# Performance work log

Measured on AMD Instinct MI355X. Metric: run time of the kernel, lower is better.

Reference implementation:

```python
import jax, jax.numpy as jnp
import numpy as np

B = 64          # batch
NV = 6890       # SMPL vertices
NF = 13776      # SMPL faces
NHD = 20000     # HD (uniformly resampled) vertices
NP = 24         # SMPL parts
COP_W = 10.0
COP_K = 100.0
EPS = 1e-6


def setup_inputs() -> dict:
    key = jax.random.key(0)
    k1, k2, k3, k4, k5 = jax.random.split(key, 5)
    vertices = jax.random.normal(k1, (B, NV, 3), jnp.float32)
    hd_operator = jax.random.uniform(k2, (NHD, NV), jnp.float32) / NV
    faces = jax.random.randint(k3, (NF, 3), 0, NV)          # triangle vertex ids
    vert_fid = jax.random.randint(k4, (NHD,), 0, NF)        # HD vert -> source face
    face_part = jax.random.randint(k5, (NF,), 0, NP)        # face -> body part
    return {"vertices": vertices, "hd_operator": hd_operator,
            "faces": faces, "vert_fid": vert_fid, "face_part": face_part}


def reference(vertices, hd_operator, faces, vert_fid, face_part):
    # --- per-part volume: signed tetrahedron volume per face, summed per part ---
    tri = vertices[:, faces]                      # [B, NF, 3, 3]
    v0, v1, v2 = tri[:, :, 0], tri[:, :, 1], tri[:, :, 2]
    vol_f = jnp.abs(jnp.einsum('bfi,bfi->bf', v0, jnp.cross(v1, v2))) / 6.0  # [B, NF]
    part_onehot = jax.nn.one_hot(face_part, NP, dtype=vol_f.dtype)           # [NF, NP]
    per_part_volume = jnp.einsum('bf,fp->bp', vol_f, part_onehot)            # [B, NP]

    vertices_hd = jnp.einsum('nm,bmd->bnd', hd_operator, vertices)           # [B, NHD, 3]

    # --- map each HD vertex to the volume of its part ---
    part_of_vert = face_part[vert_fid]                                       # [NHD]
    vol_vert = per_part_volume[:, part_of_vert][..., None]                   # [B, NHD, 1]

    # --- volume-weighted COM ---
    com = jnp.sum(vertices_hd * vol_vert, axis=1) / jnp.sum(vol_vert, axis=1)  # [B, 3]

    # --- pressure-weighted COP ---
    h = vertices_hd[:, :, 1]  # vertex height above ground plane (y)
    pw = jnp.where(h < 0.0, 1.0 - COP_K * h, jnp.exp(-COP_W * h))            # [B, NHD]
    cop = jnp.sum(vertices_hd * pw[..., None], axis=1) / (
        jnp.sum(pw, axis=1, keepdims=True) + EPS)                            # [B, 3]

    # --- stability loss: xz distance between COM and COP ---
    d = com - cop
    return jnp.sqrt(d[:, 0] ** 2 + d[:, 2] ** 2)                             # [B]
```

## Files before the change

kernel.cpp:

```cpp
#include <hip/hip_runtime.h>
#include <cstdint>

#define B_    64
#define NV_   6890
#define NF_   13776
#define NHD_  20000
#define NP_   24
#define NCH   216
#define BUF_HW 6144

#define OFF_PPV   0u
#define OFF_RED   6144u
#define OFF_VC    7680u

typedef __attribute__((ext_vector_type(8))) __bf16 bf16x8;
typedef __attribute__((ext_vector_type(4))) float f32x4;

__device__ __forceinline__ unsigned short f2bf(float f) {
    unsigned u = __float_as_uint(f);
    u = (u + 0x7fffu + ((u >> 16) & 1u)) >> 16;
    return (unsigned short)u;
}

__global__ __launch_bounds__(256) void k_init(float* __restrict__ z) {
    for (int i = threadIdx.x; i < 1920; i += 256) z[i] = 0.f;
}

__global__ __launch_bounds__(256) void k0v_pack(const float* __restrict__ verts,
                                                unsigned short* __restrict__ Vc) {
    int idx = blockIdx.x * 256 + threadIdx.x;
    int j    = idx & 7;
    int lane = (idx >> 3) & 63;
    int ct   = idx >> 9;
    int t    = ct % 12;
    int c    = ct / 12;
    int lm   = lane & 15;
    int kk   = (lane >> 4) * 8 + j;
    int bd   = t * 16 + lm;
    int d    = bd >> 6, b = bd & 63;
    int k    = c * 32 + kk;
    float v  = (k < NV_) ? verts[((size_t)b * NV_ + k) * 3 + d] : 0.f;
    Vc[idx] = f2bf(v);
}

__global__ __launch_bounds__(256) void k1_vol(const float* __restrict__ verts,
                                              const int* __restrict__ faces,
                                              const int* __restrict__ face_part,
                                              float* __restrict__ ppv) {
    __shared__ float bins[NP_];
    int b = blockIdx.y;
    int f = blockIdx.x * 256 + threadIdx.x;
    if (threadIdx.x < NP_) bins[threadIdx.x] = 0.f;
    __syncthreads();
    if (f < NF_) {
        int i0 = faces[3 * f], i1 = faces[3 * f + 1], i2 = faces[3 * f + 2];
        const float* vb = verts + (size_t)b * NV_ * 3;
        float ax = vb[3 * i0], ay = vb[3 * i0 + 1], az = vb[3 * i0 + 2];
        float bx = vb[3 * i1], by = vb[3 * i1 + 1], bz = vb[3 * i1 + 2];
        float cx = vb[3 * i2], cy = vb[3 * i2 + 1], cz = vb[3 * i2 + 2];
        float crx = by * cz - bz * cy;
        float cry = bz * cx - bx * cz;
        float crz = bx * cy - by * cx;
        float vol = fabsf(ax * crx + ay * cry + az * crz) * (1.0f / 6.0f);
        atomicAdd(&bins[face_part[f]], vol);
    }
    __syncthreads();
    if (threadIdx.x < NP_) atomicAdd(&ppv[b * NP_ + threadIdx.x], bins[threadIdx.x]);
}

__global__ __launch_bounds__(64) void kf_fused(const float* __restrict__ Hm,
                                               const unsigned short* __restrict__ Vc,
                                               const int* __restrict__ vert_fid,
                                               const int* __restrict__ face_part,
                                               const float* __restrict__ ppv,
                                               float* __restrict__ red) {
    __shared__ unsigned short Vl[2 * BUF_HW];
    const int lane = threadIdx.x;
    const int lm   = lane & 15;
    const int kg   = lane >> 4;
    const int n0   = blockIdx.x * 32;
    const float* Arow0 = Hm + (size_t)(n0 + lm) * NV_;
    const float* Arow1 = Hm + (size_t)(n0 + 16 + lm) * NV_;

    f32x4 acc0[12], acc1[12];
#pragma unroll
    for (int t = 0; t < 12; ++t) {
        acc0[t] = (f32x4){0.f, 0.f, 0.f, 0.f};
        acc1[t] = (f32x4){0.f, 0.f, 0.f, 0.f};
    }

    auto stage = [&](int cc, unsigned short* dst) {
        const unsigned short* src = Vc + (size_t)cc * BUF_HW + lane * 8;
#pragma unroll
        for (int i = 0; i < 12; ++i)
            __builtin_amdgcn_global_load_lds(
                (const __attribute__((address_space(1))) void*)(src + i * 512),
                (__attribute__((address_space(3))) void*)(dst + i * 512), 16, 0, 0);
    };
    auto loadA = [&](int cc, float2* ra, float2* rb) {
        int k0 = cc * 32 + kg * 8;
#pragma unroll
        for (int j = 0; j < 4; ++j) {
            ra[j] = *reinterpret_cast<const float2*>(Arow0 + k0 + 2 * j);
            rb[j] = *reinterpret_cast<const float2*>(Arow1 + k0 + 2 * j);
        }
    };

    stage(0, &Vl[0]);
    float2 a[4], b[4];
    loadA(0, a, b);

    int p = 0;
#pragma unroll 1
    for (int c = 0; c < NCH - 1; ++c) {
        asm volatile("s_waitcnt vmcnt(0)" ::: "memory");
        __builtin_amdgcn_sched_barrier(0);
        bf16x8 Af0, Af1;
#pragma unroll
        for (int j = 0; j < 4; ++j) {
            Af0[2 * j]     = (__bf16)a[j].x;
            Af0[2 * j + 1] = (__bf16)a[j].y;
            Af1[2 * j]     = (__bf16)b[j].x;
            Af1[2 * j + 1] = (__bf16)b[j].y;
        }
        __builtin_amdgcn_sched_barrier(0);
        stage(c + 1, &Vl[(p ^ 1) * BUF_HW]);
        int cpf = (c + 1 < NCH - 1) ? (c + 1) : (NCH - 2);
        loadA(cpf, a, b);
        __builtin_amdgcn_sched_barrier(0);
        bf16x8 Bu[12];
        const unsigned short* bp = &Vl[p * BUF_HW] + lane * 8;
#pragma unroll
        for (int t = 0; t < 12; ++t)
            Bu[t] = *reinterpret_cast<const bf16x8*>(bp + t * 512);
#pragma unroll
        for (int t = 0; t < 12; ++t)
            acc0[t] = __builtin_amdgcn_mfma_f32_16x16x32_bf16(Af0, Bu[t], acc0[t], 0, 0, 0);
#pragma unroll
        for (int t = 0; t < 12; ++t)
            acc1[t] = __builtin_amdgcn_mfma_f32_16x16x32_bf16(Af1, Bu[t], acc1[t], 0, 0, 0);
        p ^= 1;
    }

    {
        asm volatile("s_waitcnt vmcnt(0)" ::: "memory");
        __builtin_amdgcn_sched_barrier(0);
        bf16x8 Bu[12];
        const unsigned short* bp = &Vl[p * BUF_HW] + lane * 8;
#pragma unroll
        for (int t = 0; t < 12; ++t)
            Bu[t] = *reinterpret_cast<const bf16x8*>(bp + t * 512);
        int k0 = (NCH - 1) * 32 + kg * 8;
        bf16x8 Af0, Af1;
#pragma unroll
        for (int j = 0; j < 8; ++j) {
            int k = k0 + j;
            float fa = (k < NV_) ? Arow0[k] : 0.f;
            float fb = (k < NV_) ? Arow1[k] : 0.f;
            Af0[j] = (__bf16)fa;
            Af1[j] = (__bf16)fb;
        }
#pragma unroll
        for (int t = 0; t < 12; ++t)
            acc0[t] = __builtin_amdgcn_mfma_f32_16x16x32_bf16(Af0, Bu[t], acc0[t], 0, 0, 0);
#pragma unroll
        for (int t = 0; t < 12; ++t)
            acc1[t] = __builtin_amdgcn_mfma_f32_16x16x32_bf16(Af1, Bu[t], acc1[t], 0, 0, 0);
    }

    int part0[4], part1[4];
#pragma unroll
    for (int r = 0; r < 4; ++r) {
        part0[r] = face_part[vert_fid[n0 + kg * 4 + r]];
        part1[r] = face_part[vert_fid[n0 + 16 + kg * 4 + r]];
    }
    float sums[4][6];
#pragma unroll
    for (int t = 0; t < 4; ++t)
#pragma unroll
        for (int q = 0; q < 6; ++q) sums[t][q] = 0.f;

#pragma unroll
    for (int t = 0; t < 4; ++t) {
        int bcol = t * 16 + lm;
#pragma unroll
        for (int r = 0; r < 4; ++r) {
            {
                float x = acc0[t][r], h = acc0[4 + t][r], z = acc0[8 + t][r];
                float pwv = (h < 0.f) ? (1.f - 100.f * h) : expf(-10.f * h);
                float w = ppv[bcol * NP_ + part0[r]];
                sums[t][0] += pwv * x; sums[t][1] += pwv * z;
                sums[t][2] += w * x;   sums[t][3] += w * z;
                sums[t][4] += pwv;     sums[t][5] += w;
            }
            {
                float x = acc1[t][r], h = acc1[4 + t][r], z = acc1[8 + t][r];
                float pwv = (h < 0.f) ? (1.f - 100.f * h) : expf(-10.f * h);
                float w = ppv[bcol * NP_ + part1[r]];
                sums[t][0] += pwv * x; sums[t][1] += pwv * z;
                sums[t][2] += w * x;   sums[t][3] += w * z;
                sums[t][4] += pwv;     sums[t][5] += w;
            }
        }
    }
#pragma unroll
    for (int t = 0; t < 4; ++t)
#pragma unroll
        for (int q = 0; q < 6; ++q) {
            float v = sums[t][q];
            v += __shfl_xor(v, 16);
            v += __shfl_xor(v, 32);
            sums[t][q] = v;
        }
    if (kg == 0) {
#pragma unroll
        for (int t = 0; t < 4; ++t) {
            int bcol = t * 16 + lm;
#pragma unroll
            for (int q = 0; q < 6; ++q)
                atomicAdd(&red[bcol * 6 + q], sums[t][q]);
        }
    }
}

__global__ __launch_bounds__(64) void k5_final(const float* __restrict__ red,
                                               float* __restrict__ out) {
    int b = threadIdx.x;
    if (b < B_) {
        float sp   = red[b * 6 + 4] + 1e-6f;
        float sw   = red[b * 6 + 5];
        float copx = red[b * 6 + 0] / sp;
        float copz = red[b * 6 + 1] / sp;
        float comx = red[b * 6 + 2] / sw;
        float comz = red[b * 6 + 3] / sw;
        float dx = comx - copx, dz = comz - copz;
        out[b] = sqrtf(dx * dx + dz * dz);
    }
}

extern "C" void kernel_launch(void* const* d_in, const int* in_sizes, int n_in,
                              void* d_out, int out_size, void* d_ws, size_t ws_size,
                              hipStream_t stream) {
    const float* verts     = (const float*)d_in[0];
    const float* Hm        = (const float*)d_in[1];
    const int*   faces     = (const int*)d_in[2];
    const int*   vert_fid  = (const int*)d_in[3];
    const int*   face_part = (const int*)d_in[4];
    char* ws = (char*)d_ws;
    float*          ppv = (float*)(ws + OFF_PPV);
    float*          red = (float*)(ws + OFF_RED);
    unsigned short* Vc  = (unsigned short*)(ws + OFF_VC);
    float* out = (float*)d_out;

    hipLaunchKernelGGL(k_init, dim3(1), dim3(256), 0, stream, (float*)ws);
    hipLaunchKernelGGL(k0v_pack, dim3((NCH * 12 * 512) / 256), dim3(256), 0, stream, verts, Vc);
    hipLaunchKernelGGL(k1_vol, dim3(54, 64), dim3(256), 0, stream, verts, faces, face_part, ppv);
    hipLaunchKernelGGL(kf_fused, dim3(NHD_ / 32), dim3(64), 0, stream,
                       Hm, Vc, vert_fid, face_part, ppv, red);
    hipLaunchKernelGGL(k5_final, dim3(1), dim3(64), 0, stream, red, out);
}
```

Baseline: 361.1 us.

## Use 4-wave blocks with split-K and shared B tiles in fused regressor GEMM

The fused HD-regressor kernel now launches 256-thread blocks of four waves. Two waves cover 64 output rows and share the staged vertex tiles in LDS, each loading half of them. The other pair splits the K dimension in half, and the two halves' accumulators are reduced through LDS before the epilogue. This is meant to shorten each wave's serial K loop, raise the number of memory requests in flight per CU, and cut redundant B staging. In exchange it adds block-wide barriers every iteration, an LDS reduction step, and bounds masking for the partial last block.

```diff
diff --git a/kernel.cpp b/kernel.cpp
--- a/kernel.cpp
+++ b/kernel.cpp
@@ -7,6 +7,7 @@
 #define NHD_  20000
 #define NP_   24
 #define NCH   216
+#define ITERS 108
 #define BUF_HW 6144
 
 #define OFF_PPV   0u
@@ -68,19 +69,27 @@
     if (threadIdx.x < NP_) atomicAdd(&ppv[b * NP_ + threadIdx.x], bins[threadIdx.x]);
 }
 
-__global__ __launch_bounds__(64) void kf_fused(const float* __restrict__ Hm,
-                                               const unsigned short* __restrict__ Vc,
-                                               const int* __restrict__ vert_fid,
-                                               const int* __restrict__ face_part,
-                                               const float* __restrict__ ppv,
-                                               float* __restrict__ red) {
-    __shared__ unsigned short Vl[2 * BUF_HW];
-    const int lane = threadIdx.x;
+__global__ __launch_bounds__(256) void kf_fused(const float* __restrict__ Hm,
+                                                const unsigned short* __restrict__ Vc,
+                                                const int* __restrict__ vert_fid,
+                                                const int* __restrict__ face_part,
+                                                const float* __restrict__ ppv,
+                                                float* __restrict__ red) {
+    __shared__ unsigned short Vb[2][2][BUF_HW];
+    const int tid  = threadIdx.x;
+    const int lane = tid & 63;
+    const int w    = tid >> 6;
+    const int wr   = w & 1;
+    const int ws   = w >> 1;
     const int lm   = lane & 15;
     const int kg   = lane >> 4;
-    const int n0   = blockIdx.x * 32;
-    const float* Arow0 = Hm + (size_t)(n0 + lm) * NV_;
-    const float* Arow1 = Hm + (size_t)(n0 + 16 + lm) * NV_;
+    const int n0   = blockIdx.x * 64;
+    const int rowbase = n0 + 32 * wr;
+    const int r0c = min(rowbase + lm,      NHD_ - 1);
+    const int r1c = min(rowbase + 16 + lm, NHD_ - 1);
+    const float* Arow0 = Hm + (size_t)r0c * NV_;
+    const float* Arow1 = Hm + (size_t)r1c * NV_;
+    const int cbase = ws * ITERS;
 
     f32x4 acc0[12], acc1[12];
 #pragma unroll
@@ -89,31 +98,55 @@
         acc1[t] = (f32x4){0.f, 0.f, 0.f, 0.f};
     }
 
-    auto stage = [&](int cc, unsigned short* dst) {
-        const unsigned short* src = Vc + (size_t)cc * BUF_HW + lane * 8;
-#pragma unroll
-        for (int i = 0; i < 12; ++i)
+    auto stageTiles = [&](int cc, int pp) {
+        const unsigned short* src = Vc + (size_t)cc * BUF_HW;
+        unsigned short* dst = &Vb[ws][pp][0];
+#pragma unroll
+        for (int i = 0; i < 6; ++i) {
+            int t = wr * 6 + i;
             __builtin_amdgcn_global_load_lds(
-                (const __attribute__((address_space(1))) void*)(src + i * 512),
-                (__attribute__((address_space(3))) void*)(dst + i * 512), 16, 0, 0);
+                (const __attribute__((address_space(1))) void*)(src + t * 512 + lane * 8),
+                (__attribute__((address_space(3))) void*)(dst + t * 512 + lane * 8), 16, 0, 0);
+        }
     };
     auto loadA = [&](int cc, float2* ra, float2* rb) {
         int k0 = cc * 32 + kg * 8;
-#pragma unroll
-        for (int j = 0; j < 4; ++j) {
-            ra[j] = *reinterpret_cast<const float2*>(Arow0 + k0 + 2 * j);
-            rb[j] = *reinterpret_cast<const float2*>(Arow1 + k0 + 2 * j);
+        if (cc == NCH - 1) {
+            float ta[8], tb[8];
+#pragma unroll
+            for (int j = 0; j < 8; ++j) {
+                int k = k0 + j;
+                ta[j] = (k < NV_) ? Arow0[k] : 0.f;
+                tb[j] = (k < NV_) ? Arow1[k] : 0.f;
+            }
+#pragma unroll
+            for (int j = 0; j < 4; ++j) {
+                ra[j] = make_float2(ta[2 * j], ta[2 * j + 1]);
+                rb[j] = make_float2(tb[2 * j], tb[2 * j + 1]);
+            }
+        } else {
+#pragma unroll
+            for (int j = 0; j < 4; ++j) {
+                ra[j] = *reinterpret_cast<const float2*>(Arow0 + k0 + 2 * j);
+                rb[j] = *reinterpret_cast<const float2*>(Arow1 + k0 + 2 * j);
+            }
         }
     };
 
-    stage(0, &Vl[0]);
+    stageTiles(cbase, 0);
     float2 a[4], b[4];
-    loadA(0, a, b);
+    loadA(cbase, a, b);
+    __syncthreads();
 
     int p = 0;
 #pragma unroll 1
-    for (int c = 0; c < NCH - 1; ++c) {
-        asm volatile("s_waitcnt vmcnt(0)" ::: "memory");
+    for (int i = 0; i < ITERS; ++i) {
+        const int c = cbase + i;
+        bf16x8 Bu[12];
+        const unsigned short* bp = &Vb[ws][p][0] + lane * 8;
+#pragma unroll
+        for (int t = 0; t < 12; ++t)
+            Bu[t] = *reinterpret_cast<const bf16x8*>(bp + t * 512);
         __builtin_amdgcn_sched_barrier(0);
         bf16x8 Af0, Af1;
 #pragma unroll
@@ -124,101 +157,90 @@
             Af1[2 * j + 1] = (__bf16)b[j].y;
         }
         __builtin_amdgcn_sched_barrier(0);
-        stage(c + 1, &Vl[(p ^ 1) * BUF_HW]);
-        int cpf = (c + 1 < NCH - 1) ? (c + 1) : (NCH - 2);
-        loadA(cpf, a, b);
+        if (i + 1 < ITERS) stageTiles(c + 1, p ^ 1);
+        loadA((i + 1 < ITERS) ? c + 1 : c, a, b);
         __builtin_amdgcn_sched_barrier(0);
-        bf16x8 Bu[12];
-        const unsigned short* bp = &Vl[p * BUF_HW] + lane * 8;
-#pragma unroll
-        for (int t = 0; t < 12; ++t)
-            Bu[t] = *reinterpret_cast<const bf16x8*>(bp + t * 512);
 #pragma unroll
         for (int t = 0; t < 12; ++t)
             acc0[t] = __builtin_amdgcn_mfma_f32_16x16x32_bf16(Af0, Bu[t], acc0[t], 0, 0, 0);
 #pragma unroll
         for (int t = 0; t < 12; ++t)
             acc1[t] = __builtin_amdgcn_mfma_f32_16x16x32_bf16(Af1, Bu[t], acc1[t], 0, 0, 0);
+        __syncthreads();
         p ^= 1;
     }
 
-    {
-        asm volatile("s_waitcnt vmcnt(0)" ::: "memory");
-        __builtin_amdgcn_sched_barrier(0);
-        bf16x8 Bu[12];
-        const unsigned short* bp = &Vl[p * BUF_HW] + lane * 8;
-#pragma unroll
-        for (int t = 0; t < 12; ++t)
-            Bu[t] = *reinterpret_cast<const bf16x8*>(bp + t * 512);
-        int k0 = (NCH - 1) * 32 + kg * 8;
-        bf16x8 Af0, Af1;
-#pragma unroll
-        for (int j = 0; j < 8; ++j) {
-            int k = k0 + j;
-            float fa = (k < NV_) ? Arow0[k] : 0.f;
-            float fb = (k < NV_) ? Arow1[k] : 0.f;
-            Af0[j] = (__bf16)fa;
-            Af1[j] = (__bf16)fb;
-        }
-#pragma unroll
-        for (int t = 0; t < 12; ++t)
-            acc0[t] = __builtin_amdgcn_mfma_f32_16x16x32_bf16(Af0, Bu[t], acc0[t], 0, 0, 0);
-#pragma unroll
-        for (int t = 0; t < 12; ++t)
-            acc1[t] = __builtin_amdgcn_mfma_f32_16x16x32_bf16(Af1, Bu[t], acc1[t], 0, 0, 0);
-    }
-
-    int part0[4], part1[4];
-#pragma unroll
-    for (int r = 0; r < 4; ++r) {
-        part0[r] = face_part[vert_fid[n0 + kg * 4 + r]];
-        part1[r] = face_part[vert_fid[n0 + 16 + kg * 4 + r]];
-    }
-    float sums[4][6];
-#pragma unroll
-    for (int t = 0; t < 4; ++t)
-#pragma unroll
-        for (int q = 0; q < 6; ++q) sums[t][q] = 0.f;
-
-#pragma unroll
-    for (int t = 0; t < 4; ++t) {
-        int bcol = t * 16 + lm;
+    float* dump = reinterpret_cast<float*>(&Vb[0][0][0]);
+    if (ws == 1) {
+#pragma unroll
+        for (int t = 0; t < 12; ++t) {
+            *reinterpret_cast<f32x4*>(dump + wr * 6144 + (t * 64 + lane) * 4)        = acc0[t];
+            *reinterpret_cast<f32x4*>(dump + wr * 6144 + ((12 + t) * 64 + lane) * 4) = acc1[t];
+        }
+    }
+    __syncthreads();
+    if (ws == 0) {
+#pragma unroll
+        for (int t = 0; t < 12; ++t) {
+            acc0[t] += *reinterpret_cast<const f32x4*>(dump + wr * 6144 + (t * 64 + lane) * 4);
+            acc1[t] += *reinterpret_cast<const f32x4*>(dump + wr * 6144 + ((12 + t) * 64 + lane) * 4);
+        }
+        int part0[4], part1[4];
+        float val0[4], val1[4];
 #pragma unroll
         for (int r = 0; r < 4; ++r) {
-            {
-                float x = acc0[t][r], h = acc0[4 + t][r], z = acc0[8 + t][r];
-                float pwv = (h < 0.f) ? (1.f - 100.f * h) : expf(-10.f * h);
-                float w = ppv[bcol * NP_ + part0[r]];
-                sums[t][0] += pwv * x; sums[t][1] += pwv * z;
-                sums[t][2] += w * x;   sums[t][3] += w * z;
-                sums[t][4] += pwv;     sums[t][5] += w;
-            }
-            {
-                float x = acc1[t][r], h = acc1[4 + t][r], z = acc1[8 + t][r];
-                float pwv = (h < 0.f) ? (1.f - 100.f * h) : expf(-10.f * h);
-                float w = ppv[bcol * NP_ + part1[r]];
-                sums[t][0] += pwv * x; sums[t][1] += pwv * z;
-                sums[t][2] += w * x;   sums[t][3] += w * z;
-                sums[t][4] += pwv;     sums[t][5] += w;
-            }
-        }
-    }
-#pragma unroll
-    for (int t = 0; t < 4; ++t)
-#pragma unroll
-        for (int q = 0; q < 6; ++q) {
-            float v = sums[t][q];
-            v += __shfl_xor(v, 16);
-            v += __shfl_xor(v, 32);
-            sums[t][q] = v;
-        }
-    if (kg == 0) {
+            int nn0 = rowbase + kg * 4 + r;
+            int nn1 = rowbase + 16 + kg * 4 + r;
+            part0[r] = face_part[vert_fid[min(nn0, NHD_ - 1)]];
+            part1[r] = face_part[vert_fid[min(nn1, NHD_ - 1)]];
+            val0[r] = (nn0 < NHD_) ? 1.f : 0.f;
+            val1[r] = (nn1 < NHD_) ? 1.f : 0.f;
+        }
+        float sums[4][6];
+#pragma unroll
+        for (int t = 0; t < 4; ++t)
+#pragma unroll
+            for (int q = 0; q < 6; ++q) sums[t][q] = 0.f;
 #pragma unroll
         for (int t = 0; t < 4; ++t) {
             int bcol = t * 16 + lm;
 #pragma unroll
-            for (int q = 0; q < 6; ++q)
-                atomicAdd(&red[bcol * 6 + q], sums[t][q]);
+            for (int r = 0; r < 4; ++r) {
+                {
+                    float x = acc0[t][r], h = acc0[4 + t][r], z = acc0[8 + t][r];
+                    float pwv = ((h < 0.f) ? (1.f - 100.f * h) : expf(-10.f * h)) * val0[r];
+                    float wv  = ppv[bcol * NP_ + part0[r]] * val0[r];
+                    sums[t][0] += pwv * x; sums[t][1] += pwv * z;
+                    sums[t][2] += wv * x;  sums[t][3] += wv * z;
+                    sums[t][4] += pwv;     sums[t][5] += wv;
+                }
+                {
+                    float x = acc1[t][r], h = acc1[4 + t][r], z = acc1[8 + t][r];
+                    float pwv = ((h < 0.f) ? (1.f - 100.f * h) : expf(-10.f * h)) * val1[r];
+                    float wv  = ppv[bcol * NP_ + part1[r]] * val1[r];
+                    sums[t][0] += pwv * x; sums[t][1] += pwv * z;
+                    sums[t][2] += wv * x;  sums[t][3] += wv * z;
+                    sums[t][4] += pwv;     sums[t][5] += wv;
+                }
+            }
+        }
+#pragma unroll
+        for (int t = 0; t < 4; ++t)
+#pragma unroll
+            for (int q = 0; q < 6; ++q) {
+                float v = sums[t][q];
+                v += __shfl_xor(v, 16);
+                v += __shfl_xor(v, 32);
+                sums[t][q] = v;
+            }
+        if (kg == 0) {
+#pragma unroll
+            for (int t = 0; t < 4; ++t) {
+                int bcol = t * 16 + lm;
+#pragma unroll
+                for (int q = 0; q < 6; ++q)
+                    atomicAdd(&red[bcol * 6 + q], sums[t][q]);
+            }
         }
     }
 }
@@ -255,7 +277,7 @@
     hipLaunchKernelGGL(k_init, dim3(1), dim3(256), 0, stream, (float*)ws);
     hipLaunchKernelGGL(k0v_pack, dim3((NCH * 12 * 512) / 256), dim3(256), 0, stream, verts, Vc);
     hipLaunchKernelGGL(k1_vol, dim3(54, 64), dim3(256), 0, stream, verts, faces, face_part, ppv);
-    hipLaunchKernelGGL(kf_fused, dim3(NHD_ / 32), dim3(64), 0, stream,
+    hipLaunchKernelGGL(kf_fused, dim3((NHD_ + 63) / 64), dim3(256), 0, stream,
                        Hm, Vc, vert_fid, face_part, ppv, red);
     hipLaunchKernelGGL(k5_final, dim3(1), dim3(64), 0, stream, red, out);
 }
```

Measured after the change: 440.5 us. +22.0%, slower.

## Triple-buffer A and B tiles through LDS with async global-to-LDS loads

Applied to the files above, without the earlier changes.

Moves the fp32 hd_operator (A) tiles from per-lane register loads to direct global_load_lds into a swizzled LDS buffer, and deepens the pipeline from double to triple buffering so that two chunks are in flight. The wait drops from vmcnt(0) to vmcnt(16), letting the next chunk's loads overlap the current MFMA work. This is meant to hide the latency of the memory-bound A stream, at the cost of more LDS per block (which may lower occupancy) and a more intricate tail handling for the last chunks.

```diff
diff --git a/kernel.cpp b/kernel.cpp
--- a/kernel.cpp
+++ b/kernel.cpp
@@ -7,7 +7,6 @@
 #define NHD_  20000
 #define NP_   24
 #define NCH   216
-#define BUF_HW 6144
 
 #define OFF_PPV   0u
 #define OFF_RED   6144u
@@ -74,13 +73,14 @@
                                                const int* __restrict__ face_part,
                                                const float* __restrict__ ppv,
                                                float* __restrict__ red) {
-    __shared__ unsigned short Vl[2 * BUF_HW];
+    __shared__ unsigned short Bl[3][6144];
+    __shared__ float          Al[3][1024];
     const int lane = threadIdx.x;
     const int lm   = lane & 15;
     const int kg   = lane >> 4;
     const int n0   = blockIdx.x * 32;
-    const float* Arow0 = Hm + (size_t)(n0 + lm) * NV_;
-    const float* Arow1 = Hm + (size_t)(n0 + 16 + lm) * NV_;
+    const int arow = lane >> 3;
+    const int aseg = (lane & 7) ^ arow;
 
     f32x4 acc0[12], acc1[12];
 #pragma unroll
@@ -89,83 +89,115 @@
         acc1[t] = (f32x4){0.f, 0.f, 0.f, 0.f};
     }
 
-    auto stage = [&](int cc, unsigned short* dst) {
-        const unsigned short* src = Vc + (size_t)cc * BUF_HW + lane * 8;
-#pragma unroll
-        for (int i = 0; i < 12; ++i)
+    auto stageB = [&](int c, int s) {
+        const unsigned short* src = Vc + (size_t)c * 6144 + lane * 8;
+        unsigned short* dst = &Bl[s][lane * 8];
+#pragma unroll
+        for (int t = 0; t < 12; ++t)
             __builtin_amdgcn_global_load_lds(
-                (const __attribute__((address_space(1))) void*)(src + i * 512),
-                (__attribute__((address_space(3))) void*)(dst + i * 512), 16, 0, 0);
-    };
-    auto loadA = [&](int cc, float2* ra, float2* rb) {
-        int k0 = cc * 32 + kg * 8;
-#pragma unroll
-        for (int j = 0; j < 4; ++j) {
-            ra[j] = *reinterpret_cast<const float2*>(Arow0 + k0 + 2 * j);
-            rb[j] = *reinterpret_cast<const float2*>(Arow1 + k0 + 2 * j);
-        }
-    };
-
-    stage(0, &Vl[0]);
-    float2 a[4], b[4];
-    loadA(0, a, b);
-
-    int p = 0;
-#pragma unroll 1
-    for (int c = 0; c < NCH - 1; ++c) {
-        asm volatile("s_waitcnt vmcnt(0)" ::: "memory");
-        __builtin_amdgcn_sched_barrier(0);
-        bf16x8 Af0, Af1;
-#pragma unroll
-        for (int j = 0; j < 4; ++j) {
-            Af0[2 * j]     = (__bf16)a[j].x;
-            Af0[2 * j + 1] = (__bf16)a[j].y;
-            Af1[2 * j]     = (__bf16)b[j].x;
-            Af1[2 * j + 1] = (__bf16)b[j].y;
-        }
-        __builtin_amdgcn_sched_barrier(0);
-        stage(c + 1, &Vl[(p ^ 1) * BUF_HW]);
-        int cpf = (c + 1 < NCH - 1) ? (c + 1) : (NCH - 2);
-        loadA(cpf, a, b);
-        __builtin_amdgcn_sched_barrier(0);
-        bf16x8 Bu[12];
-        const unsigned short* bp = &Vl[p * BUF_HW] + lane * 8;
-#pragma unroll
-        for (int t = 0; t < 12; ++t)
-            Bu[t] = *reinterpret_cast<const bf16x8*>(bp + t * 512);
+                (const __attribute__((address_space(1))) void*)(src + t * 512),
+                (__attribute__((address_space(3))) void*)(dst + t * 512), 16, 0, 0);
+    };
+    auto stageA = [&](int c, int s) {
+#pragma unroll
+        for (int r = 0; r < 4; ++r) {
+            const float* src = Hm + (size_t)(n0 + r * 8 + arow) * NV_ + c * 32 + aseg * 4;
+            float* dst = &Al[s][r * 256 + lane * 4];
+            __builtin_amdgcn_global_load_lds(
+                (const __attribute__((address_space(1))) void*)src,
+                (__attribute__((address_space(3))) void*)dst, 16, 0, 0);
+        }
+    };
+    auto readA = [&](int s, bf16x8& Af0, bf16x8& Af1) {
+        const int x0 = ((2 * kg)     ^ (lm & 7)) * 4;
+        const int x1 = ((2 * kg + 1) ^ (lm & 7)) * 4;
+        f32x4 a0 = *(const f32x4*)&Al[s][lm * 32 + x0];
+        f32x4 a1 = *(const f32x4*)&Al[s][lm * 32 + x1];
+        f32x4 b0 = *(const f32x4*)&Al[s][(16 + lm) * 32 + x0];
+        f32x4 b1 = *(const f32x4*)&Al[s][(16 + lm) * 32 + x1];
+#pragma unroll
+        for (int w = 0; w < 4; ++w) {
+            Af0[w] = (__bf16)a0[w]; Af0[4 + w] = (__bf16)a1[w];
+            Af1[w] = (__bf16)b0[w]; Af1[4 + w] = (__bf16)b1[w];
+        }
+    };
+    auto mfma24 = [&](const bf16x8& Af0, const bf16x8& Af1, const bf16x8* Bu) {
 #pragma unroll
         for (int t = 0; t < 12; ++t)
             acc0[t] = __builtin_amdgcn_mfma_f32_16x16x32_bf16(Af0, Bu[t], acc0[t], 0, 0, 0);
 #pragma unroll
         for (int t = 0; t < 12; ++t)
             acc1[t] = __builtin_amdgcn_mfma_f32_16x16x32_bf16(Af1, Bu[t], acc1[t], 0, 0, 0);
-        p ^= 1;
+    };
+    auto step = [&](int c, int s, int s2) {
+        asm volatile("s_waitcnt vmcnt(16)" ::: "memory");
+        __builtin_amdgcn_sched_barrier(0);
+        bf16x8 Bu[12];
+        const unsigned short* bp = &Bl[s][lane * 8];
+#pragma unroll
+        for (int t = 0; t < 12; ++t) Bu[t] = *(const bf16x8*)(bp + t * 512);
+        bf16x8 Af0, Af1;
+        readA(s, Af0, Af1);
+        __builtin_amdgcn_sched_barrier(0);
+        stageB(c + 2, s2);
+        stageA(c + 2, s2);
+        __builtin_amdgcn_sched_barrier(0);
+        mfma24(Af0, Af1, Bu);
+    };
+
+    stageB(0, 0); stageA(0, 0);
+    stageB(1, 1); stageA(1, 1);
+
+#pragma unroll 1
+    for (int cc = 0; cc < 213; cc += 3) {
+        step(cc, 0, 2);
+        step(cc + 1, 1, 0);
+        step(cc + 2, 2, 1);
     }
 
     {
         asm volatile("s_waitcnt vmcnt(0)" ::: "memory");
         __builtin_amdgcn_sched_barrier(0);
         bf16x8 Bu[12];
-        const unsigned short* bp = &Vl[p * BUF_HW] + lane * 8;
-#pragma unroll
-        for (int t = 0; t < 12; ++t)
-            Bu[t] = *reinterpret_cast<const bf16x8*>(bp + t * 512);
-        int k0 = (NCH - 1) * 32 + kg * 8;
+        const unsigned short* bp = &Bl[0][lane * 8];
+#pragma unroll
+        for (int t = 0; t < 12; ++t) Bu[t] = *(const bf16x8*)(bp + t * 512);
+        bf16x8 Af0, Af1; readA(0, Af0, Af1);
+        __builtin_amdgcn_sched_barrier(0);
+        stageB(215, 2);
+        __builtin_amdgcn_sched_barrier(0);
+        mfma24(Af0, Af1, Bu);
+    }
+    {
+        asm volatile("s_waitcnt vmcnt(0)" ::: "memory");
+        __builtin_amdgcn_sched_barrier(0);
+        bf16x8 Bu[12];
+        const unsigned short* bp = &Bl[1][lane * 8];
+#pragma unroll
+        for (int t = 0; t < 12; ++t) Bu[t] = *(const bf16x8*)(bp + t * 512);
+        bf16x8 Af0, Af1; readA(1, Af0, Af1);
+        mfma24(Af0, Af1, Bu);
+    }
+    {
+        asm volatile("s_waitcnt vmcnt(0)" ::: "memory");
+        __builtin_amdgcn_sched_barrier(0);
+        bf16x8 Bu[12];
+        const unsigned short* bp = &Bl[2][lane * 8];
+#pragma unroll
+        for (int t = 0; t < 12; ++t) Bu[t] = *(const bf16x8*)(bp + t * 512);
+        const float* Arow0 = Hm + (size_t)(n0 + lm) * NV_;
+        const float* Arow1 = Hm + (size_t)(n0 + 16 + lm) * NV_;
         bf16x8 Af0, Af1;
 #pragma unroll
         for (int j = 0; j < 8; ++j) {
-            int k = k0 + j;
-            float fa = (k < NV_) ? Arow0[k] : 0.f;
-            float fb = (k < NV_) ? Arow1[k] : 0.f;
+            int ko = kg * 8 + j;
+            int k  = 6880 + ko;
+            float fa = (ko < 10) ? Arow0[k] : 0.f;
+            float fb = (ko < 10) ? Arow1[k] : 0.f;
             Af0[j] = (__bf16)fa;
             Af1[j] = (__bf16)fb;
         }
-#pragma unroll
-        for (int t = 0; t < 12; ++t)
-            acc0[t] = __builtin_amdgcn_mfma_f32_16x16x32_bf16(Af0, Bu[t], acc0[t], 0, 0, 0);
-#pragma unroll
-        for (int t = 0; t < 12; ++t)
-            acc1[t] = __builtin_amdgcn_mfma_f32_16x16x32_bf16(Af1, Bu[t], acc1[t], 0, 0, 0);
+        mfma24(Af0, Af1, Bu);
     }
 
     int part0[4], part1[4];
```

Measured after the change: 303.8 us. -15.9%, faster.
